# Performance work log

Measured on AMD Instinct MI355X. Metric: run time of the kernel, lower is better.

## Reference

```python
import jax, jax.numpy as jnp
import numpy as np

LAMBDA_VOLUME = 0.2
LAMBDA_WEIGHTED_ADJ = 0.15
LAMBDA_SYM = 0.05
AGE_MAX = 100.0
EPS_ROW = 1e-8
EPS_STD = 1e-6


def _smooth_l1(x):
    # F.smooth_l1_loss(x, 0) with beta=1, mean reduction
    ax = jnp.abs(x)
    return jnp.mean(jnp.where(ax < 1.0, 0.5 * x * x, ax - 0.5))


def setup_inputs() -> dict:
    key = jax.random.key(0)
    ks = jax.random.split(key, 9)
    B, C, X = 2, 32, 96
    logits = jax.random.normal(ks[0], (B, C, X, X, X), dtype=jnp.float32)
    age = jax.random.uniform(ks[1], (B, 1), dtype=jnp.float32) * AGE_MAX
    w_young = jax.random.uniform(ks[2], (C, C), dtype=jnp.float32)
    w_old = jax.random.uniform(ks[3], (C, C), dtype=jnp.float32)
    # expected per-class volumes ~ total_voxels / C in scale
    vol_means_young = jax.random.uniform(ks[4], (C,), dtype=jnp.float32) * 50000.0
    vol_means_old = jax.random.uniform(ks[5], (C,), dtype=jnp.float32) * 50000.0
    vol_stds_young = jax.random.uniform(ks[6], (C,), dtype=jnp.float32) * 5000.0 + 1000.0
    vol_stds_old = jax.random.uniform(ks[7], (C,), dtype=jnp.float32) * 5000.0 + 1000.0
    prior_adj = jax.random.uniform(ks[8], (C, C), dtype=jnp.float32)
    # left-right pair permutation: class i <-> i + C//2
    perm = jnp.concatenate([jnp.arange(C // 2, C), jnp.arange(0, C // 2)]).astype(jnp.int64)
    return {"logits": logits, "age": age, "w_young": w_young, "w_old": w_old,
            "vol_means_young": vol_means_young, "vol_means_old": vol_means_old,
            "vol_stds_young": vol_stds_young, "vol_stds_old": vol_stds_old,
            "prior_adj": prior_adj, "perm": perm}


def reference(logits, age, w_young, w_old, vol_means_young, vol_means_old,
              vol_stds_young, vol_stds_old, prior_adj, perm):
    B, C = logits.shape[0], logits.shape[1]
    probs = jax.nn.softmax(logits, axis=1)  # (B,C,X,Y,Z)
    alpha = jnp.clip(age / AGE_MAX, 0.0, 1.0)  # (B,1) interpolation between age anchors

    # ---- weighted adjacency loss (temperature == 1.0 -> no pow) ----
    pf = probs.reshape(B, C, -1)                     # (B,C,N)
    A = jnp.einsum('bcn,bdn->bcd', pf, pf)           # bmm(probs, probs^T)
    A = A * (1.0 - jnp.eye(C, dtype=A.dtype))        # zero diagonal
    W = (1.0 - alpha)[:, :, None] * w_young[None] + alpha[:, :, None] * w_old[None]  # (B,C,C)
    A = A * W
    Aw = A.mean(axis=0)
    Aw = Aw / jnp.clip(Aw.sum(axis=1, keepdims=True), EPS_ROW)
    prior = prior_adj * (1.0 - jnp.eye(C, dtype=prior_adj.dtype))
    prior = prior / jnp.clip(prior.sum(axis=1, keepdims=True), EPS_ROW)
    loss_adj = jnp.mean(jnp.abs(Aw - prior))

    # ---- volume consistency loss ----
    pred_vol = probs.sum(axis=(2, 3, 4))             # (B,C)
    means = (1.0 - alpha) * vol_means_young[None] + alpha * vol_means_old[None]
    stds = (1.0 - alpha) * vol_stds_young[None] + alpha * vol_stds_old[None]
    loss_vol = _smooth_l1((pred_vol - means) / (stds + EPS_STD))

    # ---- symmetry consistency loss (flip along X axis = dim 2, swap LR pairs) ----
    p_flip = jnp.flip(probs, axis=2)
    p_swap = p_flip[:, perm]                         # channel permutation = pairwise swap
    loss_sym = jnp.mean(jnp.abs(probs - p_swap))

    total = (LAMBDA_WEIGHTED_ADJ * loss_adj
             + LAMBDA_VOLUME * loss_vol
             + LAMBDA_SYM * loss_sym)
    return total
```

## Files before the change

kernel.cpp:

```cpp
#include <hip/hip_runtime.h>
#include <math.h>

#define CX 32
#define XX 9216
#define X3 884736
#define CHUNKS_PER_B 13824
#define WAVES_PER_B 2048
#define NBLOCKS 1024
#define RSU 17
#define RS16 34
#define SLICE_W 1088

typedef short s8v __attribute__((ext_vector_type(8)));
typedef float f32x16 __attribute__((ext_vector_type(16)));

__device__ __forceinline__ unsigned bf16rne(float f) {
    unsigned u = __float_as_uint(f);
    return (u + (0x7fffu + ((u >> 16) & 1u))) >> 16;
}


__global__ __launch_bounds__(256, 4)
void main_pass(const float* __restrict__ logits,
               float* __restrict__ A_acc,
               float* __restrict__ sym_acc)
{
    __shared__ __align__(16) unsigned lds_u[8704];
    const int tid = threadIdx.x;
    const int w   = tid >> 6;
    const int l   = tid & 63;
    const int wid = blockIdx.x * 4 + w;
    const int b   = wid >> 11;
    const int wb  = wid & 2047;
    const int lane31 = l & 31;
    const int h = l >> 5;

    unsigned* const buf0 = lds_u + w * (2 * SLICE_W);
    const float* lg = logits + (size_t)b * (size_t)(CX * X3);

    f32x16 acc = {};
    float sym = 0.f;

    for (int it = 0, cg = wb; cg < CHUNKS_PER_B; ++it, cg += WAVES_PER_B) {
        unsigned* const sb = buf0 + (it & 1) * SLICE_W;
        int x   = cg / 288;
        int rem = (cg - x * 288) * 32 + lane31;
        int xx  = h ? (95 - x) : x;
        const float* gp = lg + (size_t)xx * XX + (size_t)rem;

        float p[CX];
#pragma unroll
        for (int c = 0; c < CX; ++c) p[c] = gp[(size_t)c * X3];
        float m = p[0];
#pragma unroll
        for (int c = 1; c < CX; ++c) m = fmaxf(m, p[c]);
        float ssum = 0.f;
#pragma unroll
        for (int c = 0; c < CX; ++c) { p[c] = __expf(p[c] - m); ssum += p[c]; }
        float inv = 1.f / ssum;
#pragma unroll
        for (int c = 0; c < CX; ++c) p[c] *= inv;

        unsigned* myrow = sb + l * RSU;
#pragma unroll
        for (int c2 = 0; c2 < 16; ++c2)
            myrow[c2] = bf16rne(p[2 * c2]) | (bf16rne(p[2 * c2 + 1]) << 16);

        __syncthreads();

        const unsigned* prow = sb + (l ^ 32) * RSU;
#pragma unroll
        for (int j = 0; j < 16; ++j) {
            unsigned q = prow[(j + 8) & 15];
            sym += fabsf(p[2 * j]     - __uint_as_float(q << 16));
            sym += fabsf(p[2 * j + 1] - __uint_as_float(q & 0xffff0000u));
        }

        const unsigned short* sb16 = (const unsigned short*)sb;
#pragma unroll
        for (int t = 0; t < 4; ++t) {
            s8v af;
#pragma unroll
            for (int j = 0; j < 8; ++j)
                af[j] = (short)sb16[(16 * t + 8 * h + j) * RS16 + lane31];
            acc = __builtin_amdgcn_mfma_f32_32x32x16_bf16(af, af, acc, 0, 0, 0);
        }
    }

    __syncthreads();
    float* lds_f = (float*)lds_u;
#pragma unroll
    for (int r = 0; r < 16; ++r) {
        int row = (r & 3) + 8 * (r >> 2) + 4 * h;
        lds_f[w * 1056 + row * 32 + lane31] = acc[r];
    }
    float sv = sym;
#pragma unroll
    for (int o = 32; o >= 1; o >>= 1) sv += __shfl_down(sv, o);
    if (l == 0) lds_f[4224 + w] = sv;
    __syncthreads();

    {
        float4 s = make_float4(0.f, 0.f, 0.f, 0.f);
#pragma unroll
        for (int ww = 0; ww < 4; ++ww) {
            const float4 v = *((const float4*)lds_f + ww * 264 + tid);
            s.x += v.x; s.y += v.y; s.z += v.z; s.w += v.w;
        }
        float* Ab = A_acc + b * (CX * CX) + tid * 4;
        atomicAdd(&Ab[0], s.x);
        atomicAdd(&Ab[1], s.y);
        atomicAdd(&Ab[2], s.z);
        atomicAdd(&Ab[3], s.w);
    }
    if (tid == 0)
        atomicAdd(sym_acc, lds_f[4224] + lds_f[4225] + lds_f[4226] + lds_f[4227]);
}

__global__ void finalize(const float* __restrict__ A_acc,
                         const float* __restrict__ sym,
                         const float* __restrict__ age,
                         const float* __restrict__ wy,  const float* __restrict__ wo,
                         const float* __restrict__ vmy, const float* __restrict__ vmo,
                         const float* __restrict__ vsy, const float* __restrict__ vso,
                         const float* __restrict__ prior,
                         float* __restrict__ out)
{
    const int t = threadIdx.x;
    float a0 = fminf(fmaxf(age[0] * 0.01f, 0.f), 1.f);
    float a1 = fminf(fmaxf(age[1] * 0.01f, 0.f), 1.f);

    const int bb = t >> 5, c = t & 31;
    float full = 0.f;
#pragma unroll
    for (int d = 0; d < CX; ++d) full += A_acc[bb * 1024 + c * CX + d];

    float part_vol;
    {
        float al = bb ? a1 : a0;
        float mean = (1.f - al) * vmy[c] + al * vmo[c];
        float sd   = (1.f - al) * vsy[c] + al * vso[c] + 1e-6f;
        float r  = (full - mean) / sd;
        float ar = fabsf(r);
        part_vol = (ar < 1.f) ? 0.5f * r * r : (ar - 0.5f);
    }

    float part_adj = 0.f;
    if (t < 32) {
        float awrow[CX], prow[CX];
        float rs = 0.f, ps = 0.f;
#pragma unroll
        for (int d = 0; d < CX; ++d) {
            float v = 0.f, pv = 0.f;
            if (d != c) {
                float A0v = A_acc[c * CX + d];
                float A1v = A_acc[1024 + c * CX + d];
                float w0 = (1.f - a0) * wy[c * CX + d] + a0 * wo[c * CX + d];
                float w1 = (1.f - a1) * wy[c * CX + d] + a1 * wo[c * CX + d];
                v  = 0.5f * (A0v * w0 + A1v * w1);
                pv = prior[c * CX + d];
            }
            awrow[d] = v;  rs += v;
            prow[d]  = pv; ps += pv;
        }
        rs = fmaxf(rs, 1e-8f);
        ps = fmaxf(ps, 1e-8f);
#pragma unroll
        for (int d = 0; d < CX; ++d)
            part_adj += fabsf(awrow[d] / rs - prow[d] / ps);
    }

#pragma unroll
    for (int off = 32; off >= 1; off >>= 1) {
        part_adj += __shfl_down(part_adj, off);
        part_vol += __shfl_down(part_vol, off);
    }
    if (t == 0) {
        float loss_adj = part_adj * (1.f / 1024.f);
        float loss_vol = part_vol * (1.f / 64.f);
        float loss_sym = sym[0] / 56623104.f;
        out[0] = 0.15f * loss_adj + 0.2f * loss_vol + 0.05f * loss_sym;
    }
}

extern "C" void kernel_launch(void* const* d_in, const int* in_sizes, int n_in,
                              void* d_out, int out_size, void* d_ws, size_t ws_size,
                              hipStream_t stream) {
    const float* logits = (const float*)d_in[0];
    const float* age    = (const float*)d_in[1];
    const float* wy     = (const float*)d_in[2];
    const float* wo     = (const float*)d_in[3];
    const float* vmy    = (const float*)d_in[4];
    const float* vmo    = (const float*)d_in[5];
    const float* vsy    = (const float*)d_in[6];
    const float* vso    = (const float*)d_in[7];
    const float* prior  = (const float*)d_in[8];

    float* ws    = (float*)d_ws;
    float* A_acc = ws;
    float* sym   = ws + 2048;

    hipMemsetAsync(d_ws, 0, 2049 * sizeof(float), stream);
    main_pass<<<NBLOCKS, 256, 0, stream>>>(logits, A_acc, sym);
    finalize<<<1, 64, 0, stream>>>(A_acc, sym, age, wy, wo,
                                   vmy, vmo, vsy, vso, prior, (float*)d_out);
}
```

Baseline: 392.0 us.

## Prefetch next chunk into registers and replace block barrier with wave-local fence

Software-pipelines the main loop by issuing the global loads for the next chunk into a second register array before processing the current one, so load latency overlaps with the softmax and MFMA work. It also replaces the block-wide __syncthreads with a per-wave workgroup-scope release/acquire on an LDS flag, since each wave only reads its own LDS slice. The double register buffer raises VGPR pressure under launch_bounds(256,4), which may cause spills, and the fence-only sync relies on wave-lockstep semantics for LDS visibility.

```diff
diff --git a/kernel.cpp b/kernel.cpp
--- a/kernel.cpp
+++ b/kernel.cpp
@@ -19,6 +19,58 @@
     return (u + (0x7fffu + ((u >> 16) & 1u))) >> 16;
 }
 
+__device__ __forceinline__ void load_chunk(float (&p)[CX], const float* __restrict__ lg,
+                                           int cg, int lane31, int h) {
+    int x   = cg / 288;
+    int rem = (cg - x * 288) * 32 + lane31;
+    int xx  = h ? (95 - x) : x;
+    const float* gp = lg + (size_t)xx * XX + (size_t)rem;
+#pragma unroll
+    for (int c = 0; c < CX; ++c) p[c] = gp[(size_t)c * X3];
+}
+
+__device__ __forceinline__ void process_chunk(float (&p)[CX], unsigned* sb, int* flag,
+                                              f32x16& acc, float& sym,
+                                              int l, int lane31, int h) {
+    float m = p[0];
+#pragma unroll
+    for (int c = 1; c < CX; ++c) m = fmaxf(m, p[c]);
+    float ssum = 0.f;
+#pragma unroll
+    for (int c = 0; c < CX; ++c) { p[c] = __expf(p[c] - m); ssum += p[c]; }
+    float inv = 1.f / ssum;
+#pragma unroll
+    for (int c = 0; c < CX; ++c) p[c] *= inv;
+
+    unsigned* myrow = sb + l * RSU;
+#pragma unroll
+    for (int c2 = 0; c2 < 16; ++c2)
+        myrow[c2] = bf16rne(p[2 * c2]) | (bf16rne(p[2 * c2 + 1]) << 16);
+
+    __builtin_amdgcn_sched_barrier(0);
+    __hip_atomic_store(flag, 1, __ATOMIC_RELEASE, __HIP_MEMORY_SCOPE_WORKGROUP);
+    (void)__hip_atomic_load(flag, __ATOMIC_ACQUIRE, __HIP_MEMORY_SCOPE_WORKGROUP);
+    __builtin_amdgcn_sched_barrier(0);
+
+    const unsigned* prow = sb + (l ^ 32) * RSU;
+#pragma unroll
+    for (int j = 0; j < 16; ++j) {
+        unsigned q = prow[(j + 8) & 15];
+        sym += fabsf(p[2 * j]     - __uint_as_float(q << 16));
+        sym += fabsf(p[2 * j + 1] - __uint_as_float(q & 0xffff0000u));
+    }
+
+    const unsigned short* sb16 = (const unsigned short*)sb;
+#pragma unroll
+    for (int t = 0; t < 4; ++t) {
+        s8v af;
+#pragma unroll
+        for (int j = 0; j < 8; ++j)
+            af[j] = (short)sb16[(16 * t + 8 * h + j) * RS16 + lane31];
+        acc = __builtin_amdgcn_mfma_f32_32x32x16_bf16(af, af, acc, 0, 0, 0);
+    }
+}
+
 
 __global__ __launch_bounds__(256, 4)
 void main_pass(const float* __restrict__ logits,
@@ -26,6 +78,7 @@
                float* __restrict__ sym_acc)
 {
     __shared__ __align__(16) unsigned lds_u[8704];
+    __shared__ int flags[4];
     const int tid = threadIdx.x;
     const int w   = tid >> 6;
     const int l   = tid & 63;
@@ -36,54 +89,24 @@
     const int h = l >> 5;
 
     unsigned* const buf0 = lds_u + w * (2 * SLICE_W);
+    int* const flag = &flags[w];
     const float* lg = logits + (size_t)b * (size_t)(CX * X3);
 
     f32x16 acc = {};
     float sym = 0.f;
 
-    for (int it = 0, cg = wb; cg < CHUNKS_PER_B; ++it, cg += WAVES_PER_B) {
-        unsigned* const sb = buf0 + (it & 1) * SLICE_W;
-        int x   = cg / 288;
-        int rem = (cg - x * 288) * 32 + lane31;
-        int xx  = h ? (95 - x) : x;
-        const float* gp = lg + (size_t)xx * XX + (size_t)rem;
-
-        float p[CX];
-#pragma unroll
-        for (int c = 0; c < CX; ++c) p[c] = gp[(size_t)c * X3];
-        float m = p[0];
-#pragma unroll
-        for (int c = 1; c < CX; ++c) m = fmaxf(m, p[c]);
-        float ssum = 0.f;
-#pragma unroll
-        for (int c = 0; c < CX; ++c) { p[c] = __expf(p[c] - m); ssum += p[c]; }
-        float inv = 1.f / ssum;
-#pragma unroll
-        for (int c = 0; c < CX; ++c) p[c] *= inv;
-
-        unsigned* myrow = sb + l * RSU;
-#pragma unroll
-        for (int c2 = 0; c2 < 16; ++c2)
-            myrow[c2] = bf16rne(p[2 * c2]) | (bf16rne(p[2 * c2 + 1]) << 16);
-
-        __syncthreads();
-
-        const unsigned* prow = sb + (l ^ 32) * RSU;
-#pragma unroll
-        for (int j = 0; j < 16; ++j) {
-            unsigned q = prow[(j + 8) & 15];
-            sym += fabsf(p[2 * j]     - __uint_as_float(q << 16));
-            sym += fabsf(p[2 * j + 1] - __uint_as_float(q & 0xffff0000u));
-        }
-
-        const unsigned short* sb16 = (const unsigned short*)sb;
-#pragma unroll
-        for (int t = 0; t < 4; ++t) {
-            s8v af;
-#pragma unroll
-            for (int j = 0; j < 8; ++j)
-                af[j] = (short)sb16[(16 * t + 8 * h + j) * RS16 + lane31];
-            acc = __builtin_amdgcn_mfma_f32_32x32x16_bf16(af, af, acc, 0, 0, 0);
+    float pa[CX], pb[CX];
+    load_chunk(pa, lg, wb, lane31, h);
+    int it = 0;
+    for (int cur = wb; cur < CHUNKS_PER_B; cur += WAVES_PER_B, ++it) {
+        unsigned* sb = buf0 + (it & 1) * SLICE_W;
+        int nxt = cur + WAVES_PER_B;
+        if ((it & 1) == 0) {
+            if (nxt < CHUNKS_PER_B) load_chunk(pb, lg, nxt, lane31, h);
+            process_chunk(pa, sb, flag, acc, sym, l, lane31, h);
+        } else {
+            if (nxt < CHUNKS_PER_B) load_chunk(pa, lg, nxt, lane31, h);
+            process_chunk(pb, sb, flag, acc, sym, l, lane31, h);
         }
     }
 
```

New measurement: 526.2 us. +34.2%, slower.
